# Performance work log

Measured on AMD Instinct MI355X. Metric: run time of the kernel, lower is better.

## Reference

```python
import jax, jax.numpy as jnp
import numpy as np

N_NODES = 50000


def setup_inputs() -> dict:
    key = jax.random.key(0)
    ks = jax.random.split(key, 6)
    F_IN, F_HID, N_EDGES = 128, 512, 800000
    x = jax.random.normal(ks[0], (N_NODES, F_IN), dtype=jnp.float32)
    edge_index = jax.random.randint(ks[1], (2, N_EDGES), 0, N_NODES, dtype=jnp.int64)
    W1 = jax.random.normal(ks[2], (F_IN, F_HID), dtype=jnp.float32) * (1.0 / np.sqrt(F_IN))
    b1 = jnp.zeros((F_HID,), dtype=jnp.float32)
    W2 = jax.random.normal(ks[3], (F_HID, F_IN), dtype=jnp.float32) * (1.0 / np.sqrt(F_HID))
    b2 = jnp.zeros((F_IN,), dtype=jnp.float32)
    eps = jnp.zeros((), dtype=jnp.float32)  # train_eps=True, init 0
    return {"x": x, "edge_index": edge_index, "W1": W1, "b1": b1, "W2": W2, "b2": b2, "eps": eps}


def reference(x, edge_index, W1, b1, W2, b2, eps):
    # GINConv: out = MLP((1+eps)*x + sum_{j in N(i)} x_j)
    src, dst = edge_index[0], edge_index[1]
    agg = jax.ops.segment_sum(x[src], dst, num_segments=N_NODES)  # [N, F]
    h = (1.0 + eps) * x + agg
    h = jax.nn.relu(h @ W1 + b1)
    out = h @ W2 + b2
    return out
```

## Files before the change

kernel.cpp:

```cpp
#include <hip/hip_runtime.h>
#include <hip/hip_bf16.h>

#define N_NODES 50000
#define F_IN    128
#define F_HID   512
#define N_EDGES 800000

#define NBKT 782
#define RCAP 384
#define BINCAP 1280

typedef __bf16 bf16x2 __attribute__((ext_vector_type(2)));
typedef __bf16 bf16x4 __attribute__((ext_vector_type(4)));
typedef __bf16 bf16x8 __attribute__((ext_vector_type(8)));
typedef float  f32x4  __attribute__((ext_vector_type(4)));

#define NB_X 6250
#define NB_W 32
#define NB_CZ 98
__global__ __launch_bounds__(256) void prep(const float* __restrict__ x,
                                            const float* __restrict__ W1,
                                            const float* __restrict__ W2,
                                            __bf16* __restrict__ xb,
                                            __bf16* __restrict__ w1f,
                                            __bf16* __restrict__ w2f,
                                            int* __restrict__ bcnt) {
    int b = blockIdx.x, tid = threadIdx.x;
    if (b < NB_X) {
        int i = b * 256 + tid;
        float4 v = ((const float4*)x)[i];
        bf16x4 o = {(__bf16)v.x, (__bf16)v.y, (__bf16)v.z, (__bf16)v.w};
        ((bf16x4*)xb)[i] = o;
    } else if (b < NB_X + NB_W) {
        int t = (b - NB_X) * 256 + tid;
        int lane = t & 63, kk = (t >> 6) & 3, nt = (t >> 8) & 7, c = (t >> 11) & 3;
        int q = lane >> 4, l16 = lane & 15;
        bf16x8 o;
        #pragma unroll
        for (int j = 0; j < 8; ++j)
            o[j] = (__bf16)W1[(kk * 32 + q * 8 + j) * F_HID + c * 128 + nt * 16 + l16];
        *(bf16x8*)(w1f + (size_t)t * 8) = o;
    } else if (b < NB_X + 2 * NB_W) {
        int t = (b - NB_X - NB_W) * 256 + tid;
        int lane = t & 63, kk = (t >> 6) & 3, nt = (t >> 8) & 7, c = (t >> 11) & 3;
        int q = lane >> 4, l16 = lane & 15;
        bf16x8 o;
        #pragma unroll
        for (int j = 0; j < 8; ++j)
            o[j] = (__bf16)W2[(c * 128 + kk * 32 + q * 8 + j) * F_IN + nt * 16 + l16];
        *(bf16x8*)(w2f + (size_t)t * 8) = o;
    } else {
        int i = (b - NB_X - 2 * NB_W) * 256 + tid;
        if (i < NBKT * 8 * 4) {
            int4 z = {0, 0, 0, 0};
            ((int4*)bcnt)[i] = z;
        }
    }
}

__global__ __launch_bounds__(256) void bucket_fill(const int* __restrict__ ei,
                                                   int* __restrict__ bcnt,
                                                   int* __restrict__ entries) {
    int e = blockIdx.x * 256 + threadIdx.x;
    if (e >= N_EDGES) return;
    int src = ei[e];
    int dst = ei[N_EDGES + e];
    int cell = (dst >> 6) * 8 + (blockIdx.x & 7);
    int p = atomicAdd(&bcnt[cell * 16], 1);
    if (p < RCAP)
        entries[cell * RCAP + p] = ((dst & 63) << 16) | src;
}

__global__ __launch_bounds__(512) void gin_fused(const __bf16* __restrict__ xb,
                                                 const int* __restrict__ bcnt,
                                                 const int* __restrict__ entries,
                                                 const float* __restrict__ eps,
                                                 const __bf16* __restrict__ w1f,
                                                 const __bf16* __restrict__ w2f,
                                                 const float* __restrict__ b1,
                                                 const float* __restrict__ b2,
                                                 float* __restrict__ out) {
    __shared__ int degs[64], bases[64], curs[64];
    __shared__ unsigned short bin16[BINCAP];
    __shared__ __attribute__((aligned(16))) __bf16 As[8192];
    __shared__ __attribute__((aligned(16))) __bf16 Hb[8192];

    const int tid = threadIdx.x;
    const int wave = tid >> 6, lane = tid & 63;
    const int q = lane >> 4, l16 = lane & 15;
    const int bkt = blockIdx.x;

    if (tid < 64) degs[tid] = 0;
    __syncthreads();

    int cnt = bcnt[(bkt * 8 + wave) * 16];
    cnt = cnt < RCAP ? cnt : RCAP;
    const int* eb = entries + (size_t)(bkt * 8 + wave) * RCAP;
    int ev[6];
    #pragma unroll
    for (int u = 0; u < 6; ++u) {
        int i = lane + u * 64;
        int en = (i < cnt) ? eb[i] : -1;
        ev[u] = en;
        if (en >= 0) atomicAdd(&degs[en >> 16], 1);
    }
    __syncthreads();

    if (wave == 0) {
        int d = degs[lane];
        int sum = d;
        #pragma unroll
        for (int off = 1; off < 64; off <<= 1) {
            int t = __shfl_up(sum, off);
            if (lane >= off) sum += t;
        }
        bases[lane] = sum - d;
        curs[lane]  = sum - d;
    }
    __syncthreads();

    #pragma unroll
    for (int u = 0; u < 6; ++u) {
        int en = ev[u];
        if (en >= 0) {
            int p = atomicAdd(&curs[en >> 16], 1);
            if (p < BINCAP) bin16[p] = (unsigned short)(en & 0xffff);
        }
    }
    __syncthreads();

    const float s = 1.0f + eps[0];
    for (int t = 0; t < 8; ++t) {
        int n = wave * 8 + t;
        int node = bkt * 64 + n;
        if (node >= N_NODES) break;
        int dg = degs[n], b0 = bases[n];
        int end = b0 + dg;
        end = end < BINCAP ? end : BINCAP;

        float acc[8];
        #pragma unroll
        for (int i = 0; i < 8; ++i) acc[i] = 0.0f;
        if (q == 0) {
            bf16x8 self = *(const bf16x8*)(xb + (size_t)node * F_IN + l16 * 8);
            #pragma unroll
            for (int i = 0; i < 8; ++i) acc[i] = (float)self[i] * s;
        }

        int j = b0 + q;
        for (; j + 4 < end; j += 8) {
            int s0 = bin16[j];
            int s1 = bin16[j + 4];
            bf16x8 r0 = *(const bf16x8*)(xb + (size_t)s0 * F_IN + l16 * 8);
            bf16x8 r1 = *(const bf16x8*)(xb + (size_t)s1 * F_IN + l16 * 8);
            #pragma unroll
            for (int i = 0; i < 8; ++i) acc[i] += (float)r0[i] + (float)r1[i];
        }
        if (j < end) {
            bf16x8 r0 = *(const bf16x8*)(xb + (size_t)bin16[j] * F_IN + l16 * 8);
            #pragma unroll
            for (int i = 0; i < 8; ++i) acc[i] += (float)r0[i];
        }

        #pragma unroll
        for (int i = 0; i < 8; ++i) {
            acc[i] += __shfl_xor(acc[i], 16);
            acc[i] += __shfl_xor(acc[i], 32);
        }
        if (lane < 16) {
            int g = n >> 4, r16 = n & 15;
            bf16x8 o;
            #pragma unroll
            for (int i = 0; i < 8; ++i) o[i] = (__bf16)acc[i];
            int byte = (g * 16 + lane) * 256 + r16 * 16;
            byte ^= (lane & 7) << 4;
            *(bf16x8*)((char*)As + byte) = o;
        }
    }
    __syncthreads();

    const int wr = wave >> 2, wc = wave & 3;

    f32x4 acc_o[2][2];
    #pragma unroll
    for (int ni = 0; ni < 2; ++ni) {
        float bv = b2[wc * 32 + ni * 16 + l16];
        f32x4 b4 = {bv, bv, bv, bv};
        acc_o[0][ni] = b4;
        acc_o[1][ni] = b4;
    }

    for (int c = 0; c < 4; ++c) {
        f32x4 acc_h[2][2];
        #pragma unroll
        for (int ni = 0; ni < 2; ++ni) {
            float bv = b1[c * 128 + wc * 32 + ni * 16 + l16];
            f32x4 b4 = {bv, bv, bv, bv};
            acc_h[0][ni] = b4;
            acc_h[1][ni] = b4;
        }
        #pragma unroll
        for (int kk = 0; kk < 4; ++kk) {
            bf16x8 am[2], bw[2];
            #pragma unroll
            for (int mi = 0; mi < 2; ++mi) {
                int g = wr * 2 + mi;
                int byte = ((g * 4 + kk) * 4 + q) * 256 + l16 * 16;
                byte ^= ((kk * 4 + q) & 7) << 4;
                am[mi] = *(const bf16x8*)((const char*)As + byte);
            }
            #pragma unroll
            for (int ni = 0; ni < 2; ++ni)
                bw[ni] = *(const bf16x8*)(w1f +
                    ((size_t)((c * 8 + wc * 2 + ni) * 4 + kk) << 9) + lane * 8);
            #pragma unroll
            for (int mi = 0; mi < 2; ++mi)
                #pragma unroll
                for (int ni = 0; ni < 2; ++ni)
                    acc_h[mi][ni] = __builtin_amdgcn_mfma_f32_16x16x32_bf16(
                        am[mi], bw[ni], acc_h[mi][ni], 0, 0, 0);
        }
        #pragma unroll
        for (int mi = 0; mi < 2; ++mi) {
            int g = wr * 2 + mi;
            #pragma unroll
            for (int ni = 0; ni < 2; ++ni)
                #pragma unroll
                for (int r = 0; r < 4; ++r)
                    Hb[(((g * 4 + wc) * 64 + (ni * 2 + (l16 >> 3)) * 16 + q * 4 + r) << 3)
                       + (l16 & 7)] = (__bf16)fmaxf(acc_h[mi][ni][r], 0.0f);
        }
        __syncthreads();

        #pragma unroll
        for (int kk = 0; kk < 4; ++kk) {
            bf16x8 am[2], bw[2];
            #pragma unroll
            for (int mi = 0; mi < 2; ++mi)
                am[mi] = *(const bf16x8*)&Hb[(((wr * 2 + mi) * 4 + kk) * 64 + lane) << 3];
            #pragma unroll
            for (int ni = 0; ni < 2; ++ni)
                bw[ni] = *(const bf16x8*)(w2f +
                    ((size_t)((c * 8 + wc * 2 + ni) * 4 + kk) << 9) + lane * 8);
            #pragma unroll
            for (int mi = 0; mi < 2; ++mi)
                #pragma unroll
                for (int ni = 0; ni < 2; ++ni)
                    acc_o[mi][ni] = __builtin_amdgcn_mfma_f32_16x16x32_bf16(
                        am[mi], bw[ni], acc_o[mi][ni], 0, 0, 0);
        }
        __syncthreads();
    }

    const int m0 = bkt * 64;
    #pragma unroll
    for (int mi = 0; mi < 2; ++mi)
        #pragma unroll
        for (int ni = 0; ni < 2; ++ni)
            #pragma unroll
            for (int r = 0; r < 4; ++r) {
                int m = m0 + wr * 32 + mi * 16 + q * 4 + r;
                if (m < N_NODES)
                    out[(size_t)m * F_IN + wc * 32 + ni * 16 + l16] = acc_o[mi][ni][r];
            }
}

extern "C" void kernel_launch(void* const* d_in, const int* in_sizes, int n_in,
                              void* d_out, int out_size, void* d_ws, size_t ws_size,
                              hipStream_t stream) {
    const float* x   = (const float*)d_in[0];
    const int*   ei  = (const int*)d_in[1];
    const float* W1  = (const float*)d_in[2];
    const float* b1  = (const float*)d_in[3];
    const float* W2  = (const float*)d_in[4];
    const float* b2  = (const float*)d_in[5];
    const float* eps = (const float*)d_in[6];
    float* out = (float*)d_out;

    char* ws = (char*)d_ws;
    __bf16* xb   = (__bf16*)ws;
    __bf16* w1f  = (__bf16*)(ws + 12800000);
    __bf16* w2f  = (__bf16*)(ws + 13000000);
    int*    bcnt = (int*)(ws + 13200000);
    int*    entries = (int*)(ws + 13700000);

    prep<<<NB_X + 2 * NB_W + NB_CZ, 256, 0, stream>>>(x, W1, W2, xb, w1f, w2f, bcnt);
    bucket_fill<<<(N_EDGES + 255) / 256, 256, 0, stream>>>(ei, bcnt, entries);
    gin_fused<<<NBKT, 512, 0, stream>>>(xb, bcnt, entries, eps, w1f, w2f, b1, b2, out);
}
```

Baseline: 187.4 us.

## Fuse bucket fill into prep kernel and simplify per-node binning with fixed slots

```diff
diff --git a/kernel.cpp b/kernel.cpp
--- a/kernel.cpp
+++ b/kernel.cpp
@@ -7,32 +7,44 @@
 #define N_EDGES 800000
 
 #define NBKT 782
-#define RCAP 384
-#define BINCAP 1280
+#define NREP 16
+#define RCAP 128
+#define NDMAX 64
 
 typedef __bf16 bf16x2 __attribute__((ext_vector_type(2)));
 typedef __bf16 bf16x4 __attribute__((ext_vector_type(4)));
 typedef __bf16 bf16x8 __attribute__((ext_vector_type(8)));
 typedef float  f32x4  __attribute__((ext_vector_type(4)));
-
+typedef unsigned short u16x8 __attribute__((ext_vector_type(8)));
+
+#define NB_E 3125
 #define NB_X 6250
 #define NB_W 32
-#define NB_CZ 98
-__global__ __launch_bounds__(256) void prep(const float* __restrict__ x,
-                                            const float* __restrict__ W1,
-                                            const float* __restrict__ W2,
-                                            __bf16* __restrict__ xb,
-                                            __bf16* __restrict__ w1f,
-                                            __bf16* __restrict__ w2f,
-                                            int* __restrict__ bcnt) {
+__global__ __launch_bounds__(256) void prep_fill(const float* __restrict__ x,
+                                                 const int* __restrict__ ei,
+                                                 const float* __restrict__ W1,
+                                                 const float* __restrict__ W2,
+                                                 __bf16* __restrict__ xb,
+                                                 __bf16* __restrict__ w1f,
+                                                 __bf16* __restrict__ w2f,
+                                                 int* __restrict__ bcnt,
+                                                 int* __restrict__ entries) {
     int b = blockIdx.x, tid = threadIdx.x;
-    if (b < NB_X) {
-        int i = b * 256 + tid;
+    if (b < NB_E) {
+        int e = b * 256 + tid;
+        int src = ei[e];
+        int dst = ei[N_EDGES + e];
+        int cell = (dst >> 6) * NREP + (b & (NREP - 1));
+        int p = atomicAdd(&bcnt[cell * 16], 1);
+        if (p < RCAP)
+            entries[(size_t)cell * RCAP + p] = ((dst & 63) << 16) | src;
+    } else if (b < NB_E + NB_X) {
+        int i = (b - NB_E) * 256 + tid;
         float4 v = ((const float4*)x)[i];
         bf16x4 o = {(__bf16)v.x, (__bf16)v.y, (__bf16)v.z, (__bf16)v.w};
         ((bf16x4*)xb)[i] = o;
-    } else if (b < NB_X + NB_W) {
-        int t = (b - NB_X) * 256 + tid;
+    } else if (b < NB_E + NB_X + NB_W) {
+        int t = (b - NB_E - NB_X) * 256 + tid;
         int lane = t & 63, kk = (t >> 6) & 3, nt = (t >> 8) & 7, c = (t >> 11) & 3;
         int q = lane >> 4, l16 = lane & 15;
         bf16x8 o;
@@ -40,8 +52,8 @@
         for (int j = 0; j < 8; ++j)
             o[j] = (__bf16)W1[(kk * 32 + q * 8 + j) * F_HID + c * 128 + nt * 16 + l16];
         *(bf16x8*)(w1f + (size_t)t * 8) = o;
-    } else if (b < NB_X + 2 * NB_W) {
-        int t = (b - NB_X - NB_W) * 256 + tid;
+    } else {
+        int t = (b - NB_E - NB_X - NB_W) * 256 + tid;
         int lane = t & 63, kk = (t >> 6) & 3, nt = (t >> 8) & 7, c = (t >> 11) & 3;
         int q = lane >> 4, l16 = lane & 15;
         bf16x8 o;
@@ -49,39 +61,20 @@
         for (int j = 0; j < 8; ++j)
             o[j] = (__bf16)W2[(c * 128 + kk * 32 + q * 8 + j) * F_IN + nt * 16 + l16];
         *(bf16x8*)(w2f + (size_t)t * 8) = o;
-    } else {
-        int i = (b - NB_X - 2 * NB_W) * 256 + tid;
-        if (i < NBKT * 8 * 4) {
-            int4 z = {0, 0, 0, 0};
-            ((int4*)bcnt)[i] = z;
-        }
     }
 }
 
-__global__ __launch_bounds__(256) void bucket_fill(const int* __restrict__ ei,
-                                                   int* __restrict__ bcnt,
-                                                   int* __restrict__ entries) {
-    int e = blockIdx.x * 256 + threadIdx.x;
-    if (e >= N_EDGES) return;
-    int src = ei[e];
-    int dst = ei[N_EDGES + e];
-    int cell = (dst >> 6) * 8 + (blockIdx.x & 7);
-    int p = atomicAdd(&bcnt[cell * 16], 1);
-    if (p < RCAP)
-        entries[cell * RCAP + p] = ((dst & 63) << 16) | src;
-}
-
-__global__ __launch_bounds__(512) void gin_fused(const __bf16* __restrict__ xb,
-                                                 const int* __restrict__ bcnt,
-                                                 const int* __restrict__ entries,
-                                                 const float* __restrict__ eps,
-                                                 const __bf16* __restrict__ w1f,
-                                                 const __bf16* __restrict__ w2f,
-                                                 const float* __restrict__ b1,
-                                                 const float* __restrict__ b2,
-                                                 float* __restrict__ out) {
-    __shared__ int degs[64], bases[64], curs[64];
-    __shared__ unsigned short bin16[BINCAP];
+__global__ __launch_bounds__(512, 6) void gin_fused(const __bf16* __restrict__ xb,
+                                                    const int* __restrict__ bcnt,
+                                                    const int* __restrict__ entries,
+                                                    const float* __restrict__ eps,
+                                                    const __bf16* __restrict__ w1f,
+                                                    const __bf16* __restrict__ w2f,
+                                                    const float* __restrict__ b1,
+                                                    const float* __restrict__ b2,
+                                                    float* __restrict__ out) {
+    __shared__ int degs[64];
+    __shared__ __attribute__((aligned(16))) unsigned short bin16[64 * NDMAX];
     __shared__ __attribute__((aligned(16))) __bf16 As[8192];
     __shared__ __attribute__((aligned(16))) __bf16 Hb[8192];
 
@@ -93,73 +86,58 @@
     if (tid < 64) degs[tid] = 0;
     __syncthreads();
 
-    int cnt = bcnt[(bkt * 8 + wave) * 16];
-    cnt = cnt < RCAP ? cnt : RCAP;
-    const int* eb = entries + (size_t)(bkt * 8 + wave) * RCAP;
-    int ev[6];
     #pragma unroll
-    for (int u = 0; u < 6; ++u) {
-        int i = lane + u * 64;
-        int en = (i < cnt) ? eb[i] : -1;
-        ev[u] = en;
-        if (en >= 0) atomicAdd(&degs[en >> 16], 1);
+    for (int cc = 0; cc < 2; ++cc) {
+        int cell = bkt * NREP + wave * 2 + cc;
+        int cnt = bcnt[cell * 16];
+        cnt = cnt < RCAP ? cnt : RCAP;
+        const int* eb = entries + (size_t)cell * RCAP;
+        for (int i = lane; i < cnt; i += 64) {
+            int en = eb[i];
+            int dl = en >> 16;
+            int p = atomicAdd(&degs[dl], 1);
+            if (p < NDMAX)
+                bin16[dl * NDMAX + (p & 3) * 16 + (p >> 2)] = (unsigned short)(en & 0xffff);
+        }
     }
     __syncthreads();
 
-    if (wave == 0) {
-        int d = degs[lane];
-        int sum = d;
-        #pragma unroll
-        for (int off = 1; off < 64; off <<= 1) {
-            int t = __shfl_up(sum, off);
-            if (lane >= off) sum += t;
-        }
-        bases[lane] = sum - d;
-        curs[lane]  = sum - d;
-    }
-    __syncthreads();
-
-    #pragma unroll
-    for (int u = 0; u < 6; ++u) {
-        int en = ev[u];
-        if (en >= 0) {
-            int p = atomicAdd(&curs[en >> 16], 1);
-            if (p < BINCAP) bin16[p] = (unsigned short)(en & 0xffff);
-        }
-    }
-    __syncthreads();
-
     const float s = 1.0f + eps[0];
+    const __bf16 z0 = (__bf16)0.0f;
+    const bf16x8 Z8 = {z0, z0, z0, z0, z0, z0, z0, z0};
+#define ROW(idx) (*(const bf16x8*)(xb + (size_t)(idx) * F_IN + l16 * 8))
+#define IDX(u) ((u) < 8 ? I0[(u) & 7] : I1[(u) & 7])
     for (int t = 0; t < 8; ++t) {
         int n = wave * 8 + t;
         int node = bkt * 64 + n;
         if (node >= N_NODES) break;
-        int dg = degs[n], b0 = bases[n];
-        int end = b0 + dg;
-        end = end < BINCAP ? end : BINCAP;
+        int dg = degs[n];
+        dg = dg < NDMAX ? dg : NDMAX;
+        int myc = (dg + 3 - q) >> 2;
+        u16x8 I0 = *(const u16x8*)&bin16[n * NDMAX + q * 16];
+        u16x8 I1 = *(const u16x8*)&bin16[n * NDMAX + q * 16 + 8];
 
         float acc[8];
         #pragma unroll
         for (int i = 0; i < 8; ++i) acc[i] = 0.0f;
         if (q == 0) {
-            bf16x8 self = *(const bf16x8*)(xb + (size_t)node * F_IN + l16 * 8);
+            bf16x8 self = ROW(node);
             #pragma unroll
             for (int i = 0; i < 8; ++i) acc[i] = (float)self[i] * s;
         }
 
-        int j = b0 + q;
-        for (; j + 4 < end; j += 8) {
-            int s0 = bin16[j];
-            int s1 = bin16[j + 4];
-            bf16x8 r0 = *(const bf16x8*)(xb + (size_t)s0 * F_IN + l16 * 8);
-            bf16x8 r1 = *(const bf16x8*)(xb + (size_t)s1 * F_IN + l16 * 8);
-            #pragma unroll
-            for (int i = 0; i < 8; ++i) acc[i] += (float)r0[i] + (float)r1[i];
-        }
-        if (j < end) {
-            bf16x8 r0 = *(const bf16x8*)(xb + (size_t)bin16[j] * F_IN + l16 * 8);
-            #pragma unroll
-            for (int i = 0; i < 8; ++i) acc[i] += (float)r0[i];
+        #pragma unroll
+        for (int u0 = 0; u0 < 16; u0 += 4) {
+            if (myc > u0) {
+                bf16x8 r0 = Z8, r1 = Z8, r2 = Z8, r3 = Z8;
+                r0 = ROW(IDX(u0));
+                if (myc > u0 + 1) r1 = ROW(IDX(u0 + 1));
+                if (myc > u0 + 2) r2 = ROW(IDX(u0 + 2));
+                if (myc > u0 + 3) r3 = ROW(IDX(u0 + 3));
+                #pragma unroll
+                for (int i = 0; i < 8; ++i)
+                    acc[i] += ((float)r0[i] + (float)r1[i]) + ((float)r2[i] + (float)r3[i]);
+            }
         }
 
         #pragma unroll
@@ -282,9 +260,10 @@
     __bf16* w1f  = (__bf16*)(ws + 12800000);
     __bf16* w2f  = (__bf16*)(ws + 13000000);
     int*    bcnt = (int*)(ws + 13200000);
-    int*    entries = (int*)(ws + 13700000);
-
-    prep<<<NB_X + 2 * NB_W + NB_CZ, 256, 0, stream>>>(x, W1, W2, xb, w1f, w2f, bcnt);
-    bucket_fill<<<(N_EDGES + 255) / 256, 256, 0, stream>>>(ei, bcnt, entries);
+    int*    entries = (int*)(ws + 14100000);
+
+    hipMemsetAsync(bcnt, 0, NBKT * NREP * 64, stream);
+    prep_fill<<<NB_E + NB_X + 2 * NB_W, 256, 0, stream>>>(x, ei, W1, W2,
+                                                          xb, w1f, w2f, bcnt, entries);
     gin_fused<<<NBKT, 512, 0, stream>>>(xb, bcnt, entries, eps, w1f, w2f, b1, b2, out);
 }
```

Result: slower. 215.6 us (+15.0%).
